# Kernel tuning notes

Hardware: AMD Instinct MI355X
Metric: run time of the kernel (lower is better)

Reference implementation:

```python
import jax, jax.numpy as jnp
import numpy as np

OBS_LEN, PRED_LEN, N, P = 8, 12, 4096, 32
EH, DH, EMB, BOT, NZ = 64, 128, 64, 1024, 8


def setup_inputs() -> dict:
    key = jax.random.key(0)
    ks = iter(jax.random.split(key, 64))
    rn = lambda shp, s=0.05: (jax.random.normal(next(ks), shp, jnp.float32) * s)
    d = {
        'obs_traj': rn((OBS_LEN, N, 2), 1.0),
        'obs_traj_rel': rn((OBS_LEN, N, 2), 0.5),
        'obs_speed': jax.random.uniform(next(ks), (OBS_LEN, N, 1), jnp.float32),
        'noise': rn((N, NZ), 1.0),
        'enc_emb_W': rn((2, EMB)), 'enc_emb_b': jnp.zeros((EMB,), jnp.float32),
        'enc_Wih': rn((EMB, 4 * EH)), 'enc_Whh': rn((EH, 4 * EH)), 'enc_b': jnp.zeros((4 * EH,), jnp.float32),
        'pool_sp_W': rn((2, 64)), 'pool_sp_b': jnp.zeros((64,), jnp.float32),
        'pool_spd_W': rn((1, 64)), 'pool_spd_b': jnp.zeros((64,), jnp.float32),
        'pool_l1_W': rn((192, 512)), 'pool_l1_b': jnp.zeros((512,), jnp.float32),
        'pool_bn1_g': jnp.ones((512,), jnp.float32), 'pool_bn1_b': jnp.zeros((512,), jnp.float32),
        'pool_l2_W': rn((512, BOT)), 'pool_l2_b': jnp.zeros((BOT,), jnp.float32),
        'pool_bn2_g': jnp.ones((BOT,), jnp.float32), 'pool_bn2_b': jnp.zeros((BOT,), jnp.float32),
        'spd_emb_W': rn((OBS_LEN, 64)), 'spd_emb_b': jnp.zeros((64,), jnp.float32),
        'ctx_l1_W': rn((EH + BOT + 64, 1024)), 'ctx_l1_b': jnp.zeros((1024,), jnp.float32),
        'ctx_bn1_g': jnp.ones((1024,), jnp.float32), 'ctx_bn1_b': jnp.zeros((1024,), jnp.float32),
        'ctx_l2_W': rn((1024, DH - NZ)), 'ctx_l2_b': jnp.zeros((DH - NZ,), jnp.float32),
        'ctx_bn2_g': jnp.ones((DH - NZ,), jnp.float32), 'ctx_bn2_b': jnp.zeros((DH - NZ,), jnp.float32),
        'dec_emb_W': rn((3, EMB)), 'dec_emb_b': jnp.zeros((EMB,), jnp.float32),
        'dec_Wih': rn((EMB, 4 * DH)), 'dec_Whh': rn((DH, 4 * DH)), 'dec_b': jnp.zeros((4 * DH,), jnp.float32),
        'h2p_W': rn((DH, 2)), 'h2p_b': jnp.zeros((2,), jnp.float32),
        'group_size': P,
    }
    return d


def _lstm(xs, Wih, Whh, b, h0, c0):
    # xs: [T, B, in]; PyTorch gate order (i, f, g, o)
    def step(carry, x):
        h, c = carry
        g = x @ Wih + h @ Whh + b
        i, f, gg, o = jnp.split(g, 4, axis=-1)
        c = jax.nn.sigmoid(f) * c + jax.nn.sigmoid(i) * jnp.tanh(gg)
        h = jax.nn.sigmoid(o) * jnp.tanh(c)
        return (h, c), h
    (h, c), _ = jax.lax.scan(step, (h0, c0), xs)
    return h, c


def _bn(x, g, b):
    # BatchNorm1d, eval mode with running_mean=0, running_var=1
    return x * g + b


def reference(obs_traj, obs_traj_rel, obs_speed, noise,
              enc_emb_W, enc_emb_b, enc_Wih, enc_Whh, enc_b,
              pool_sp_W, pool_sp_b, pool_spd_W, pool_spd_b,
              pool_l1_W, pool_l1_b, pool_bn1_g, pool_bn1_b,
              pool_l2_W, pool_l2_b, pool_bn2_g, pool_bn2_b,
              spd_emb_W, spd_emb_b,
              ctx_l1_W, ctx_l1_b, ctx_bn1_g, ctx_bn1_b,
              ctx_l2_W, ctx_l2_b, ctx_bn2_g, ctx_bn2_b,
              dec_emb_W, dec_emb_b, dec_Wih, dec_Whh, dec_b,
              h2p_W, h2p_b, group_size):
    n = obs_traj.shape[1]
    G = n // group_size
    # ---- Encoder: embed rel traj, run LSTM, take final hidden ----
    emb = obs_traj_rel @ enc_emb_W + enc_emb_b                       # [T, N, 64]
    h0 = jnp.zeros((n, EH), emb.dtype)
    final_h, _ = _lstm(emb, enc_Wih, enc_Whh, enc_b, h0, h0)         # [N, 64]
    # ---- PoolHiddenNet (vectorized per-group P x P social pooling) ----
    end_pos = obs_traj[-1].reshape(G, group_size, 2)                 # [G, P, 2]
    end_spd = obs_speed[-1].reshape(G, group_size, 1)                # [G, P, 1]
    hG = final_h.reshape(G, group_size, EH)                          # [G, P, 64]
    # rel[g, i, j] = pos[g, j] - pos[g, i]
    rel = end_pos[:, None, :, :] - end_pos[:, :, None, :]            # [G, P, P, 2]
    rel_e = rel @ pool_sp_W + pool_sp_b                              # [G, P, P, 64]
    spd_e = end_spd @ pool_spd_W + pool_spd_b                        # [G, P, 64]
    Pn = group_size
    feat = jnp.concatenate([
        rel_e,
        jnp.broadcast_to(hG[:, None, :, :], (G, Pn, Pn, EH)),
        jnp.broadcast_to(spd_e[:, None, :, :], (G, Pn, Pn, 64)),
    ], axis=-1)                                                      # [G, P, P, 192]
    h1 = jax.nn.relu(_bn(feat @ pool_l1_W + pool_l1_b, pool_bn1_g, pool_bn1_b))
    h2 = jax.nn.relu(_bn(h1 @ pool_l2_W + pool_l2_b, pool_bn2_g, pool_bn2_b))
    pool_h = jnp.max(h2, axis=2).reshape(n, BOT)                     # max over j -> [N, 1024]
    # ---- speed context: sigmoid(Linear(8 -> 64)) over obs speed history ----
    spd_hist = jnp.transpose(obs_speed[:, :, 0])                     # [N, 8]
    speed_ctx = jax.nn.sigmoid(spd_hist @ spd_emb_W + spd_emb_b)     # [N, 64]
    # ---- mlp_decoder_context + ped-level noise ----
    ctx_in = jnp.concatenate([final_h, pool_h, speed_ctx], axis=1)   # [N, 1152]
    c1 = jax.nn.relu(_bn(ctx_in @ ctx_l1_W + ctx_l1_b, ctx_bn1_g, ctx_bn1_b))
    ctx = jax.nn.relu(_bn(c1 @ ctx_l2_W + ctx_l2_b, ctx_bn2_g, ctx_bn2_b))  # [N, 120]
    dec_h = jnp.concatenate([ctx, noise], axis=1)                    # [N, 128]
    dec_c = jnp.zeros_like(dec_h)
    # ---- Decoder rollout (pred_len steps) ----
    last_pos = obs_traj[-1]
    last_speed = obs_speed[-1]                                       # [N, 1]
    x0 = jnp.concatenate([obs_traj_rel[-1], last_speed], axis=1) @ dec_emb_W + dec_emb_b

    def step(carry, _):
        h, c, x, lp = carry
        g = x @ dec_Wih + h @ dec_Whh + dec_b
        i, f, gg, o = jnp.split(g, 4, axis=-1)
        c = jax.nn.sigmoid(f) * c + jax.nn.sigmoid(i) * jnp.tanh(gg)
        h = jax.nn.sigmoid(o) * jnp.tanh(c)
        rel_pos = h @ h2p_W + h2p_b                                  # [N, 2]
        cur = rel_pos + lp
        x = jnp.concatenate([rel_pos, last_speed], axis=1) @ dec_emb_W + dec_emb_b
        return (h, c, x, cur), rel_pos

    _, rels = jax.lax.scan(step, (dec_h, dec_c, x0, last_pos), None, length=PRED_LEN)
    return rels  # [pred_len, N, 2]
```

## Files before the change

### kernel.cpp

```cpp
#include <hip/hip_runtime.h>

typedef __attribute__((ext_vector_type(8))) short v8s;
typedef __attribute__((ext_vector_type(4))) float v4f;
typedef unsigned short u16;

#define DINL static __device__ __forceinline__

DINL float b2f(u16 u){ union { unsigned uu; float ff; } x; x.uu = ((unsigned)u)<<16; return x.ff; }
DINL u16 f2b(float f){ union { float ff; unsigned uu; } x; x.ff = f; unsigned r = x.uu + 0x7FFFu + ((x.uu>>16)&1u); return (u16)(r>>16); }
DINL u16 f2b_hu(float f){ union { float ff; unsigned uu; } x; x.ff = f; return (u16)((x.uu + 0x8000u)>>16); }
DINL float sigm(float x){ return 1.0f/(1.0f+__expf(-x)); }
DINL float tanh_(float x){ return 2.0f/(1.0f+__expf(-2.0f*x)) - 1.0f; }
DINL float ld(const void* p, int i, int isf){
    return isf ? ((const float*)p)[i] : b2f(((const u16*)p)[i]);
}
DINL void g2lds16(const u16* g, u16* l){
    __builtin_amdgcn_global_load_lds(
        (const __attribute__((address_space(1))) unsigned int*)g,
        (__attribute__((address_space(3))) unsigned int*)l, 16, 0, 0);
}
DINL int detect_isf(const void* obs_speed){
    const u16* p = (const u16*)obs_speed;
    int f = 0;
    for (int i = 0; i < 16; ++i){
        u16 v = p[2*i];
        if ((v & 0x8000u) || v > 0x3F80u) f = 1;
    }
    return f;
}

#define FLAG_OFF 0x000000
#define AUX_OFF  0x000100
#define ENCF_OFF 0x010000
#define DECF_OFF 0x020000
#define CW2T_OFF 0x050000
#define W2T_OFF  0x090000
#define DECH_OFF 0x090000
#define CW1T_OFF 0x190000
#define IT_OFF   0x3D0000
#define IR_OFF   0x3F0000
#define IS_OFF   0x410000
#define INZ_OFF  0x420000
#define IW1H_OFF 0x430000
#define SM_OFF   0x440000
#define CTX_OFF  0x450000
#define AV_OFF   0xD50000
#define BIG_NEED 0x1550000

#define SM_EEW 0
#define SM_EEB 128
#define SM_ENB 192
#define SM_DEW 448
#define SM_DEB 640
#define SM_DNB 704
#define SM_H2W 1216
#define SM_H2B 1472
#define SM_SEW 1536
#define SM_SEB 2048

DINL void trans_tile(const void* in, u16* out, int K, int N, int isf,
                     int bx, int by, int t, float tile[64][65])
{
    const int nbase = bx*64, kbase = by*64;
    const int c = t & 63, r0 = (t >> 6)*16;
    for (int rep = 0; rep < 16; ++rep){
        int r = r0 + rep;
        int n = nbase + c;
        float v = 0.f;
        if (n < N) v = ld(in, (kbase + r)*N + n, isf);
        tile[r][c] = v;
    }
    __syncthreads();
    for (int rep = 0; rep < 16; ++rep){
        int r = r0 + rep;
        out[(size_t)(nbase + r)*K + kbase + c] = f2b(tile[c][r]);
    }
}

__global__ __launch_bounds__(256) void k_prep(
    const void* obs_traj, const void* obs_rel, const void* obs_speed, const void* noise,
    const void* eeW, const void* eeB, const void* enc_Wih, const void* enc_Whh, const void* encB,
    const void* spW, const void* spB, const void* spdW, const void* spdB,
    const void* pool_l1_W, const void* l1B, const void* bn1g, const void* bn1b,
    const void* pool_l2_W, const void* l2b, const void* bn2g, const void* bn2b,
    const void* seW, const void* seB,
    const void* ctx_l1_W, const void* c1b, const void* cbn1g, const void* cbn1b,
    const void* ctx_l2_W, const void* c2b, const void* cbn2g, const void* cbn2b,
    const void* deW, const void* deB, const void* dec_Wih, const void* dec_Whh, const void* decB,
    const void* h2W, const void* h2B,
    int* flag, float* AUX,
    u16* IT, u16* IR, u16* IS, u16* INZ, u16* IW1H, u16* SM,
    u16* W2T, u16* cW1T, u16* cW2T, u16* encF, u16* decF)
{
    __shared__ float tile[64][65];
    __shared__ int sisf;
    const int t = threadIdx.x;
    if (t == 0){
        int f = detect_isf(obs_speed);
        sisf = f;
        if (blockIdx.x == 0) *flag = f;
    }
    __syncthreads();
    const int isf = sisf;
    int bid = blockIdx.x;
    if (bid < 905){
        int idx = bid*256 + t;
        if (idx < 65536){ IT[idx] = f2b(ld(obs_traj, idx, isf)); return; }
        idx -= 65536;
        if (idx < 65536){ IR[idx] = f2b(ld(obs_rel, idx, isf)); return; }
        idx -= 65536;
        if (idx < 32768){ IS[idx] = f2b(ld(obs_speed, idx, isf)); return; }
        idx -= 32768;
        if (idx < 32768){ INZ[idx] = f2b(ld(noise, idx, isf)); return; }
        idx -= 32768;
        if (idx < 32768){ IW1H[idx] = f2b(ld(pool_l1_W, idx + 32768, isf)); return; }
        idx -= 32768;
        if (idx < 128){ SM[SM_EEW + idx] = f2b(ld(eeW, idx, isf)); return; }
        idx -= 128;
        if (idx < 64){ SM[SM_EEB + idx] = f2b(ld(eeB, idx, isf)); return; }
        idx -= 64;
        if (idx < 256){ SM[SM_ENB + idx] = f2b(ld(encB, idx, isf)); return; }
        idx -= 256;
        if (idx < 192){ SM[SM_DEW + idx] = f2b(ld(deW, idx, isf)); return; }
        idx -= 192;
        if (idx < 64){ SM[SM_DEB + idx] = f2b(ld(deB, idx, isf)); return; }
        idx -= 64;
        if (idx < 512){ SM[SM_DNB + idx] = f2b(ld(decB, idx, isf)); return; }
        idx -= 512;
        if (idx < 256){ SM[SM_H2W + idx] = f2b(ld(h2W, idx, isf)); return; }
        idx -= 256;
        if (idx < 2){ SM[SM_H2B + idx] = f2b(ld(h2B, idx, isf)); return; }
        idx -= 2;
        if (idx < 512){ SM[SM_SEW + idx] = f2b(ld(seW, idx, isf)); return; }
        idx -= 512;
        if (idx < 64){ SM[SM_SEB + idx] = f2b(ld(seB, idx, isf)); return; }
        return;
    }
    bid -= 905;
    if (bid < 512){
        int idx = bid*256 + t;
        if (idx < 32768){
            int jj = idx&7, lane = (idx>>3)&63, kcnf = idx>>9;
            int kc = kcnf&3, nf = kcnf>>2;
            int k = kc*32 + (lane>>4)*8 + jj, n = nf*16 + (lane&15);
            encF[idx] = (k < 64) ? f2b(ld(enc_Wih, k*256+n, isf)) : f2b(ld(enc_Whh, (k-64)*256+n, isf));
        } else {
            idx -= 32768;
            int jj = idx&7, lane = (idx>>3)&63, kcnf = idx>>9;
            int kc = kcnf % 6, nf = kcnf / 6;
            int k = kc*32 + (lane>>4)*8 + jj, n = nf*16 + (lane&15);
            decF[idx] = (k < 64) ? f2b(ld(dec_Wih, k*512+n, isf)) : f2b(ld(dec_Whh, (k-64)*512+n, isf));
        }
        return;
    }
    bid -= 512;
    if (bid < 128){ trans_tile(pool_l2_W, W2T, 512, 1024, isf, bid & 15, bid >> 4, t, tile); return; }
    bid -= 128;
    if (bid < 288){ trans_tile(ctx_l1_W, cW1T, 1152, 1024, isf, bid & 15, bid >> 4, t, tile); return; }
    bid -= 288;
    if (bid < 32){ trans_tile(ctx_l2_W, cW2T, 1024, 120, isf, bid & 1, bid >> 1, t, tile); return; }
    bid -= 32;
    {
        int idx = bid*256 + t;
        if (idx < 512){
            int c = idx;
            float m0 = 0.f, m1 = 0.f, qv = 0.f, cv = 0.f;
            for (int e = 0; e < 64; ++e){
                float w1a = ld(pool_l1_W, e*512 + c, isf);
                m0 += ld(spW, e, isf)*w1a;
                m1 += ld(spW, 64+e, isf)*w1a;
                cv += ld(spB, e, isf)*w1a;
                float w1c = ld(pool_l1_W, (128+e)*512 + c, isf);
                qv += ld(spdW, e, isf)*w1c;
                cv += ld(spdB, e, isf)*w1c;
            }
            cv += ld(l1B, c, isf);
            float g1 = ld(bn1g, c, isf), bb1 = ld(bn1b, c, isf);
            AUX[c] = m0; AUX[512+c] = m1; AUX[1024+c] = qv; AUX[1536+c] = cv;
            AUX[2048+c] = g1; AUX[2560+c] = bb1;
            AUX[3072+c] = g1*m0; AUX[3584+c] = g1*m1;
            return;
        }
        idx -= 512;
        if (idx < 1024){
            float g = ld(bn2g, idx, isf);
            AUX[4096+idx] = g; AUX[5120+idx] = ld(l2b, idx, isf)*g + ld(bn2b, idx, isf);
            return;
        }
        idx -= 1024;
        if (idx < 1024){
            float g = ld(cbn1g, idx, isf);
            AUX[6144+idx] = g; AUX[7168+idx] = ld(c1b, idx, isf)*g + ld(cbn1b, idx, isf);
            return;
        }
        idx -= 1024;
        if (idx < 128){
            int c = idx;
            float g  = (c < 120) ? ld(cbn2g, c, isf) : 1.f;
            float bb = (c < 120) ? (ld(c2b, c, isf)*g + ld(cbn2b, c, isf)) : 0.f;
            AUX[8192+c] = g; AUX[8320+c] = bb;
        }
    }
}

__global__ __launch_bounds__(256) void k_encoder(
    const u16* __restrict__ rel, const u16* __restrict__ embW, const u16* __restrict__ embB,
    const u16* __restrict__ encF, const u16* __restrict__ encB,
    const u16* __restrict__ IT, const u16* __restrict__ IS, const u16* __restrict__ IW1H,
    const u16* __restrict__ sW, const u16* __restrict__ sB,
    const float* __restrict__ AUX,
    u16* __restrict__ ctxIn, u16* __restrict__ Avec)
{
    __shared__ __align__(16) u16 Als[16*136];
    __shared__ float pxs[16], pys[16], sps[16];
    const int t = threadIdx.x, pedbase = blockIdx.x*16;
    const int w = t>>6, lane = t&63, quad = lane>>4, l15 = lane&15;
    for (int idx = t; idx < 16*64; idx += 256){ int p = idx>>6, jj = idx&63; Als[p*136 + 64 + jj] = 0; }
    if (t < 16){
        pxs[t] = b2f(IT[7*8192 + (pedbase+t)*2 + 0]);
        pys[t] = b2f(IT[7*8192 + (pedbase+t)*2 + 1]);
        sps[t] = b2f(IS[7*4096 + pedbase + t]);
    }
    {
        int p = t>>4, e0 = (t&15)*4;
        float rx = b2f(rel[(pedbase+p)*2 + 0]);
        float ry = b2f(rel[(pedbase+p)*2 + 1]);
        for (int e = e0; e < e0+4; ++e)
            Als[p*136 + e] = f2b(rx*b2f(embW[e]) + ry*b2f(embW[64+e]) + b2f(embB[e]));
    }
    const int j = w*16 + l15;
    const float bi = b2f(encB[j]), bff = b2f(encB[64+j]), bg = b2f(encB[128+j]), bo = b2f(encB[192+j]);
    float c4[4] = {0.f,0.f,0.f,0.f};
    for (int step = 0; step < 8; ++step){
        __syncthreads();
        v4f acc[4];
        for (int q = 0; q < 4; ++q) acc[q] = (v4f){0.f,0.f,0.f,0.f};
        for (int kc = 0; kc < 4; ++kc){
            v8s a = *(const v8s*)&Als[l15*136 + kc*32 + quad*8];
            for (int q = 0; q < 4; ++q){
                int nf = q*4 + w;
                v8s b = *(const v8s*)&encF[((nf*4 + kc)*64 + lane)*8];
                acc[q] = __builtin_amdgcn_mfma_f32_16x16x32_bf16(a, b, acc[q], 0, 0, 0);
            }
        }
        __syncthreads();
        for (int r = 0; r < 4; ++r){
            float gi = sigm(acc[0][r] + bi), gf = sigm(acc[1][r] + bff);
            float gg = tanh_(acc[2][r] + bg), go = sigm(acc[3][r] + bo);
            c4[r] = gf*c4[r] + gi*gg;
            Als[(quad*4 + r)*136 + 64 + j] = f2b(go*tanh_(c4[r]));
        }
        if (step < 7){
            int p = t>>4, e0 = (t&15)*4;
            float rx = b2f(rel[(step+1)*8192 + (pedbase+p)*2 + 0]);
            float ry = b2f(rel[(step+1)*8192 + (pedbase+p)*2 + 1]);
            for (int e = e0; e < e0+4; ++e)
                Als[p*136 + e] = f2b(rx*b2f(embW[e]) + ry*b2f(embW[64+e]) + b2f(embB[e]));
        }
    }
    __syncthreads();
    for (int idx = t; idx < 1024; idx += 256){
        int p = idx>>6, e = idx&63;
        ctxIn[(size_t)(pedbase+p)*1152 + e] = Als[p*136 + 64 + e];
    }
    {
        const int c0 = (t&127)*4, pg = (t>>7)*8;
        float4 acc[8];
        for (int p = 0; p < 8; ++p) acc[p] = make_float4(0.f,0.f,0.f,0.f);
        for (int e = 0; e < 64; ++e){
            ushort4 wv = *(const ushort4*)(IW1H + e*512 + c0);
            float w0 = b2f(wv.x), w1 = b2f(wv.y), w2 = b2f(wv.z), w3 = b2f(wv.w);
            for (int p = 0; p < 8; ++p){
                float h = b2f(Als[(pg+p)*136 + 64 + e]);
                acc[p].x += h*w0; acc[p].y += h*w1; acc[p].z += h*w2; acc[p].w += h*w3;
            }
        }
        float4 m0 = *(const float4*)(AUX + c0),        m1 = *(const float4*)(AUX + 512 + c0);
        float4 qv = *(const float4*)(AUX + 1024 + c0), cv = *(const float4*)(AUX + 1536 + c0);
        float4 g1 = *(const float4*)(AUX + 2048 + c0), bb = *(const float4*)(AUX + 2560 + c0);
        for (int p = 0; p < 8; ++p){
            float px = pxs[pg+p], py = pys[pg+p], sp = sps[pg+p];
            ushort4 o;
            o.x = f2b(g1.x*(px*m0.x + py*m1.x + sp*qv.x + cv.x + acc[p].x) + bb.x);
            o.y = f2b(g1.y*(px*m0.y + py*m1.y + sp*qv.y + cv.y + acc[p].y) + bb.y);
            o.z = f2b(g1.z*(px*m0.z + py*m1.z + sp*qv.z + cv.z + acc[p].z) + bb.z);
            o.w = f2b(g1.w*(px*m0.w + py*m1.w + sp*qv.w + cv.w + acc[p].w) + bb.w);
            *(ushort4*)&Avec[(size_t)(pedbase+pg+p)*512 + c0] = o;
        }
    }
    {
        int s = t & 63;
        for (int rep = 0; rep < 4; ++rep){
            int p = (t>>6)*4 + rep;
            int nid = pedbase + p;
            float a = b2f(sB[s]);
            for (int tt = 0; tt < 8; ++tt) a += b2f(IS[tt*4096 + nid]) * b2f(sW[tt*64 + s]);
            ctxIn[(size_t)nid*1152 + 1088 + s] = f2b(sigm(a));
        }
    }
}

__global__ __launch_bounds__(256, 2) void k_pool(
    const u16* __restrict__ Avec, const u16* __restrict__ W2T,
    const u16* __restrict__ IT, const float* __restrict__ AUX,
    u16* __restrict__ ctxIn)
{
    __shared__ __align__(16) u16 H1[64*512];
    __shared__ __align__(16) u16 Bls[128*64];
    const int t = threadIdx.x;
    const int g = blockIdx.x >> 4, ip = blockIdx.x & 15;
    const int w = t>>6, lane = t&63, quad = lane>>4, l15 = lane&15;
    const int aj = t>>3, ao = t&7;
    const float px0 = b2f(IT[7*8192 + (g*32 + ip*2 + 0)*2 + 0]);
    const float py0 = b2f(IT[7*8192 + (g*32 + ip*2 + 0)*2 + 1]);
    const float px1 = b2f(IT[7*8192 + (g*32 + ip*2 + 1)*2 + 0]);
    const float py1 = b2f(IT[7*8192 + (g*32 + ip*2 + 1)*2 + 1]);
    const float* M0G = AUX + 3072;
    const float* M1G = AUX + 3584;
    const u16* arow = Avec + (size_t)(g*32 + aj)*512 + ao*8;
    #pragma unroll
    for (int ch = 0; ch < 8; ++ch){
        union { v8s v; u16 u[8]; } av;
        av.v = *(const v8s*)(arow + ch*64);
        float a0[8], m0a[8], m1a[8];
        *(float4*)(m0a)   = *(const float4*)&M0G[ch*64 + ao*8];
        *(float4*)(m0a+4) = *(const float4*)&M0G[ch*64 + ao*8 + 4];
        *(float4*)(m1a)   = *(const float4*)&M1G[ch*64 + ao*8];
        *(float4*)(m1a+4) = *(const float4*)&M1G[ch*64 + ao*8 + 4];
        for (int i = 0; i < 8; ++i) a0[i] = b2f(av.u[i]);
        #pragma unroll
        for (int il = 0; il < 2; ++il){
            const float npx = (il == 0) ? -px0 : -px1;
            const float npy = (il == 0) ? -py0 : -py1;
            int r = il*32 + aj;
            int slot = (ch*8 + ao) ^ (r & 7);
            union { v8s v; u16 u[8]; } pk;
            for (int i = 0; i < 8; ++i){
                float v = __builtin_fmaf(npy, m1a[i], __builtin_fmaf(npx, m0a[i], a0[i]));
                pk.u[i] = f2b_hu(fmaxf(v, 0.f));
            }
            *(v8s*)&H1[r*512 + slot*8] = pk.v;
        }
    }
    const u16* bsrc = W2T + (size_t)(w*8 + (lane>>3))*512 + (size_t)((lane&7) ^ (lane>>3))*8;
    u16* bdst = &Bls[w*512];
    const float* S2 = AUX + 4096;
    const float* B2 = AUX + 5120;
    __syncthreads();
    for (int ntile = 0; ntile < 8; ++ntile){
        v4f acc[4][2];
        for (int mf = 0; mf < 4; ++mf) for (int nf = 0; nf < 2; ++nf) acc[mf][nf] = (v4f){0.f,0.f,0.f,0.f};
        const u16* bsn = bsrc + (size_t)ntile*128*512;
        for (int ch = 0; ch < 8; ++ch){
            __syncthreads();
            #pragma unroll
            for (int it = 0; it < 4; ++it)
                g2lds16(bsn + it*16384 + ch*64, bdst + it*2048);
            __syncthreads();
            #pragma unroll
            for (int kc = 0; kc < 2; ++kc){
                const int cgl = kc*4 + quad;
                v8s af[4];
                #pragma unroll
                for (int mf = 0; mf < 4; ++mf){
                    int r = mf*16 + l15;
                    int slot = ch*8 + (cgl ^ (l15 & 7));
                    af[mf] = *(const v8s*)&H1[r*512 + slot*8];
                }
                const int bslot = cgl ^ (l15 & 7);
                #pragma unroll
                for (int nf = 0; nf < 2; ++nf){
                    int col = w*32 + nf*16 + l15;
                    v8s bf = *(const v8s*)&Bls[col*64 + bslot*8];
                    acc[0][nf] = __builtin_amdgcn_mfma_f32_16x16x32_bf16(af[0], bf, acc[0][nf], 0, 0, 0);
                    acc[1][nf] = __builtin_amdgcn_mfma_f32_16x16x32_bf16(af[1], bf, acc[1][nf], 0, 0, 0);
                    acc[2][nf] = __builtin_amdgcn_mfma_f32_16x16x32_bf16(af[2], bf, acc[2][nf], 0, 0, 0);
                    acc[3][nf] = __builtin_amdgcn_mfma_f32_16x16x32_bf16(af[3], bf, acc[3][nf], 0, 0, 0);
                }
            }
        }
        for (int nf = 0; nf < 2; ++nf){
            int n = ntile*128 + w*32 + nf*16 + l15;
            float s = S2[n], bb = B2[n];
            float mm0 = 0.f, mm1 = 0.f;
            for (int mf = 0; mf < 2; ++mf) for (int r = 0; r < 4; ++r) mm0 = fmaxf(mm0, fmaxf(s*acc[mf][nf][r] + bb, 0.f));
            for (int mf = 2; mf < 4; ++mf) for (int r = 0; r < 4; ++r) mm1 = fmaxf(mm1, fmaxf(s*acc[mf][nf][r] + bb, 0.f));
            mm0 = fmaxf(mm0, __shfl_xor(mm0, 16)); mm0 = fmaxf(mm0, __shfl_xor(mm0, 32));
            mm1 = fmaxf(mm1, __shfl_xor(mm1, 16)); mm1 = fmaxf(mm1, __shfl_xor(mm1, 32));
            if (quad == 0) ctxIn[(size_t)(g*32 + ip*2 + 0)*1152 + 64 + n] = f2b(mm0);
            if (quad == 1) ctxIn[(size_t)(g*32 + ip*2 + 1)*1152 + 64 + n] = f2b(mm1);
        }
    }
}

template<int MF>
__global__ __launch_bounds__(256) void k_gemm_bt(
    const u16* __restrict__ A, int lda, const u16* __restrict__ BT,
    const float* __restrict__ S, const float* __restrict__ Bb,
    u16* __restrict__ out, int ldo, int K, int validN,
    const u16* __restrict__ noisep)
{
    __shared__ __align__(16) u16 Als[MF*32*72];
    __shared__ __align__(16) u16 Bls[128*72];
    const int t = threadIdx.x;
    const int m0 = blockIdx.x*(MF*32), n0 = blockIdx.y*128;
    const int w = t>>6, lane = t&63, quad = lane>>4, l15 = lane&15;
    const int rw = w>>1, cw = w&1;
    v4f acc[MF][4];
    for (int mf = 0; mf < MF; ++mf) for (int nf = 0; nf < 4; ++nf) acc[mf][nf] = (v4f){0.f,0.f,0.f,0.f};
    const int nch = K >> 6;
    for (int ch = 0; ch < nch; ++ch){
        const int k0 = ch*64;
        __syncthreads();
        if (MF == 4){
            const int srow = t>>1, sh = t&1;
            const u16* srcA = A + (size_t)(m0+srow)*lda + k0 + sh*32;
            u16* dstA = &Als[srow*72 + sh*32];
            ((v8s*)dstA)[0] = ((const v8s*)srcA)[0];
            ((v8s*)dstA)[1] = ((const v8s*)srcA)[1];
            ((v8s*)dstA)[2] = ((const v8s*)srcA)[2];
            ((v8s*)dstA)[3] = ((const v8s*)srcA)[3];
        } else {
            const int srow = t>>2, sh = t&3;
            const u16* srcA = A + (size_t)(m0+srow)*lda + k0 + sh*16;
            u16* dstA = &Als[srow*72 + sh*16];
            ((v8s*)dstA)[0] = ((const v8s*)srcA)[0];
            ((v8s*)dstA)[1] = ((const v8s*)srcA)[1];
        }
        {
            const int srow = t>>1, sh = t&1;
            const u16* srcB = BT + (size_t)(n0+srow)*K + k0 + sh*32;
            u16* dstB = &Bls[srow*72 + sh*32];
            ((v8s*)dstB)[0] = ((const v8s*)srcB)[0];
            ((v8s*)dstB)[1] = ((const v8s*)srcB)[1];
            ((v8s*)dstB)[2] = ((const v8s*)srcB)[2];
            ((v8s*)dstB)[3] = ((const v8s*)srcB)[3];
        }
        __syncthreads();
        for (int kc = 0; kc < 2; ++kc){
            v8s af[MF], bf[4];
            for (int mf = 0; mf < MF; ++mf) af[mf] = *(const v8s*)&Als[(rw*(MF*16) + mf*16 + l15)*72 + kc*32 + quad*8];
            for (int nf = 0; nf < 4; ++nf) bf[nf] = *(const v8s*)&Bls[(cw*64 + nf*16 + l15)*72 + kc*32 + quad*8];
            for (int mf = 0; mf < MF; ++mf)
                for (int nf = 0; nf < 4; ++nf)
                    acc[mf][nf] = __builtin_amdgcn_mfma_f32_16x16x32_bf16(af[mf], bf[nf], acc[mf][nf], 0, 0, 0);
        }
    }
    for (int nf = 0; nf < 4; ++nf){
        int n = n0 + cw*64 + nf*16 + l15;
        bool okn = (n < validN);
        float s = okn ? S[n] : 0.f, bb = okn ? Bb[n] : 0.f;
        bool okz = (!okn) && (noisep != nullptr) && (n < 128);
        for (int mf = 0; mf < MF; ++mf){
            int m = m0 + rw*(MF*16) + mf*16 + quad*4;
            for (int r = 0; r < 4; ++r){
                float v = fmaxf(s*acc[mf][nf][r] + bb, 0.f);
                if (okn) out[(size_t)(m+r)*ldo + n] = f2b(v);
                else if (okz) out[(size_t)(m+r)*ldo + n] = noisep[(size_t)(m+r)*8 + (n - 120)];
            }
        }
    }
}

__global__ __launch_bounds__(256) void k_decoder(
    const u16* __restrict__ decH0, const u16* __restrict__ decF, const u16* __restrict__ decB,
    const u16* __restrict__ dembW, const u16* __restrict__ dembB,
    const u16* __restrict__ h2pW, const u16* __restrict__ h2pB,
    const u16* __restrict__ obs_rel, const u16* __restrict__ obs_speed,
    const int* __restrict__ flag, void* __restrict__ outp)
{
    __shared__ __align__(16) u16 Als[16*200];
    __shared__ float rps[16][2];
    __shared__ float sps[16];
    __shared__ float h2ps[256];
    const int t = threadIdx.x, pedbase = blockIdx.x*16;
    const int w = t>>6, lane = t&63, quad = lane>>4, l15 = lane&15;
    const int isf = *flag;
    for (int idx = t; idx < 2048; idx += 256){
        int p = idx>>7, jj = idx&127;
        Als[p*200 + 64 + jj] = decH0[(pedbase+p)*128 + jj];
    }
    h2ps[t] = b2f(h2pW[t]);
    if (t < 16) sps[t] = b2f(obs_speed[7*4096 + pedbase + t]);
    if (t < 32){ int p = t>>1, cmp = t&1; rps[p][cmp] = b2f(obs_rel[7*8192 + (pedbase+p)*2 + cmp]); }
    __syncthreads();
    {
        int p = t>>4, e0 = (t&15)*4;
        for (int e = e0; e < e0+4; ++e){
            float v = rps[p][0]*b2f(dembW[e]) + rps[p][1]*b2f(dembW[64+e]) + sps[p]*b2f(dembW[128+e]) + b2f(dembB[e]);
            Als[p*200 + e] = f2b(v);
        }
    }
    float bI[2], bF[2], bG[2], bO[2];
    for (int nfl = 0; nfl < 2; ++nfl){
        int j = w*32 + nfl*16 + l15;
        bI[nfl] = b2f(decB[j]); bF[nfl] = b2f(decB[128+j]);
        bG[nfl] = b2f(decB[256+j]); bO[nfl] = b2f(decB[384+j]);
    }
    float c8[2][4] = {{0.f,0.f,0.f,0.f},{0.f,0.f,0.f,0.f}};
    for (int s = 0; s < 12; ++s){
        __syncthreads();
        v4f acc[4][2];
        for (int q = 0; q < 4; ++q) for (int nfl = 0; nfl < 2; ++nfl) acc[q][nfl] = (v4f){0.f,0.f,0.f,0.f};
        for (int kc = 0; kc < 6; ++kc){
            v8s a = *(const v8s*)&Als[l15*200 + kc*32 + quad*8];
            for (int q = 0; q < 4; ++q){
                for (int nfl = 0; nfl < 2; ++nfl){
                    int nf = q*8 + w*2 + nfl;
                    v8s b = *(const v8s*)&decF[((nf*6 + kc)*64 + lane)*8];
                    acc[q][nfl] = __builtin_amdgcn_mfma_f32_16x16x32_bf16(a, b, acc[q][nfl], 0, 0, 0);
                }
            }
        }
        __syncthreads();
        for (int nfl = 0; nfl < 2; ++nfl){
            int j = w*32 + nfl*16 + l15;
            for (int r = 0; r < 4; ++r){
                float gi = sigm(acc[0][nfl][r] + bI[nfl]), gf = sigm(acc[1][nfl][r] + bF[nfl]);
                float gg = tanh_(acc[2][nfl][r] + bG[nfl]), go = sigm(acc[3][nfl][r] + bO[nfl]);
                c8[nfl][r] = gf*c8[nfl][r] + gi*gg;
                Als[(quad*4 + r)*200 + 64 + j] = f2b(go*tanh_(c8[nfl][r]));
            }
        }
        __syncthreads();
        {
            int p = t>>4, cmp = (t>>3)&1, part = t&7;
            float rp = 0.f;
            int j0 = part*16;
            for (int jj = j0; jj < j0+16; ++jj)
                rp += b2f(Als[p*200 + 64 + jj]) * h2ps[jj*2 + cmp];
            rp += __shfl_xor(rp, 1);
            rp += __shfl_xor(rp, 2);
            rp += __shfl_xor(rp, 4);
            if (part == 0){
                rp += b2f(h2pB[cmp]);
                int oi = s*8192 + (pedbase+p)*2 + cmp;
                if (isf) ((float*)outp)[oi] = rp;
                else     ((u16*)outp)[oi]   = f2b(rp);
                rps[p][cmp] = rp;
            }
        }
        __syncthreads();
        {
            int p = t>>4, e0 = (t&15)*4;
            for (int e = e0; e < e0+4; ++e){
                float v = rps[p][0]*b2f(dembW[e]) + rps[p][1]*b2f(dembW[64+e]) + sps[p]*b2f(dembW[128+e]) + b2f(dembB[e]);
                Als[p*200 + e] = f2b(v);
            }
        }
    }
}

extern "C" void kernel_launch(void* const* d_in, const int* in_sizes, int n_in,
                              void* d_out, int out_size, void* d_ws, size_t ws_size,
                              hipStream_t stream)
{
    (void)in_sizes; (void)n_in; (void)out_size;
    const void* obs_traj  = d_in[0];
    const void* obs_rel   = d_in[1];
    const void* obs_speed = d_in[2];
    const void* noise     = d_in[3];
    const void* enc_emb_W = d_in[4];
    const void* enc_emb_b = d_in[5];
    const void* enc_Wih   = d_in[6];
    const void* enc_Whh   = d_in[7];
    const void* enc_b     = d_in[8];
    const void* pool_sp_W = d_in[9];
    const void* pool_sp_b = d_in[10];
    const void* pool_spd_W= d_in[11];
    const void* pool_spd_b= d_in[12];
    const void* pool_l1_W = d_in[13];
    const void* pool_l1_b = d_in[14];
    const void* pool_bn1_g= d_in[15];
    const void* pool_bn1_b= d_in[16];
    const void* pool_l2_W = d_in[17];
    const void* pool_l2_b = d_in[18];
    const void* pool_bn2_g= d_in[19];
    const void* pool_bn2_b= d_in[20];
    const void* spd_emb_W = d_in[21];
    const void* spd_emb_b = d_in[22];
    const void* ctx_l1_W  = d_in[23];
    const void* ctx_l1_b  = d_in[24];
    const void* ctx_bn1_g = d_in[25];
    const void* ctx_bn1_b = d_in[26];
    const void* ctx_l2_W  = d_in[27];
    const void* ctx_l2_b  = d_in[28];
    const void* ctx_bn2_g = d_in[29];
    const void* ctx_bn2_b = d_in[30];
    const void* dec_emb_W = d_in[31];
    const void* dec_emb_b = d_in[32];
    const void* dec_Wih   = d_in[33];
    const void* dec_Whh   = d_in[34];
    const void* dec_b     = d_in[35];
    const void* h2p_W     = d_in[36];
    const void* h2p_b     = d_in[37];

    char* ws = (char*)d_ws;
    int*   flag  = (int*)  (ws + FLAG_OFF);
    float* AUX   = (float*)(ws + AUX_OFF);
    u16*   encF  = (u16*)  (ws + ENCF_OFF);
    u16*   decF  = (u16*)  (ws + DECF_OFF);
    u16*   cW2T  = (u16*)  (ws + CW2T_OFF);
    u16*   W2T   = (u16*)  (ws + W2T_OFF);
    u16*   decH  = (u16*)  (ws + DECH_OFF);
    u16*   cW1T  = (u16*)  (ws + CW1T_OFF);
    u16*   IT    = (u16*)  (ws + IT_OFF);
    u16*   IR    = (u16*)  (ws + IR_OFF);
    u16*   IS    = (u16*)  (ws + IS_OFF);
    u16*   INZ   = (u16*)  (ws + INZ_OFF);
    u16*   IW1H  = (u16*)  (ws + IW1H_OFF);
    u16*   SM    = (u16*)  (ws + SM_OFF);
    u16*   ctxIn = (u16*)  (ws + CTX_OFF);
    u16*   Avec  = (u16*)  (ws + AV_OFF);
    u16*   c1    = (u16*)  (ws + AV_OFF);
    const bool big = (ws_size >= (size_t)BIG_NEED);

    k_prep<<<dim3(1876), dim3(256), 0, stream>>>(
        obs_traj, obs_rel, obs_speed, noise,
        enc_emb_W, enc_emb_b, enc_Wih, enc_Whh, enc_b,
        pool_sp_W, pool_sp_b, pool_spd_W, pool_spd_b,
        pool_l1_W, pool_l1_b, pool_bn1_g, pool_bn1_b,
        pool_l2_W, pool_l2_b, pool_bn2_g, pool_bn2_b,
        spd_emb_W, spd_emb_b,
        ctx_l1_W, ctx_l1_b, ctx_bn1_g, ctx_bn1_b,
        ctx_l2_W, ctx_l2_b, ctx_bn2_g, ctx_bn2_b,
        dec_emb_W, dec_emb_b, dec_Wih, dec_Whh, dec_b,
        h2p_W, h2p_b,
        flag, AUX, IT, IR, IS, INZ, IW1H, SM,
        W2T, cW1T, cW2T, encF, decF);
    k_encoder<<<dim3(256), dim3(256), 0, stream>>>(
        IR, SM + SM_EEW, SM + SM_EEB, encF, SM + SM_ENB,
        IT, IS, IW1H, SM + SM_SEW, SM + SM_SEB, AUX, ctxIn, Avec);
    k_pool<<<dim3(2048), dim3(256), 0, stream>>>(Avec, W2T, IT, AUX, ctxIn);
    if (big){
        k_gemm_bt<4><<<dim3(32, 8), dim3(256), 0, stream>>>(
            ctxIn, 1152, cW1T, AUX + 6144, AUX + 7168, c1, 1024, 1152, 1024, (const u16*)nullptr);
        k_gemm_bt<2><<<dim3(64, 1), dim3(256), 0, stream>>>(
            c1, 1024, cW2T, AUX + 8192, AUX + 8320, decH, 128, 1024, 120, INZ);
    } else {
        k_gemm_bt<4><<<dim3(16, 8), dim3(256), 0, stream>>>(
            ctxIn, 1152, cW1T, AUX + 6144, AUX + 7168, c1, 1024, 1152, 1024, (const u16*)nullptr);
        k_gemm_bt<2><<<dim3(32, 1), dim3(256), 0, stream>>>(
            c1, 1024, cW2T, AUX + 8192, AUX + 8320, decH, 128, 1024, 120, INZ);
        k_gemm_bt<4><<<dim3(16, 8), dim3(256), 0, stream>>>(
            ctxIn + (size_t)2048*1152, 1152, cW1T, AUX + 6144, AUX + 7168, c1, 1024, 1152, 1024, (const u16*)nullptr);
        k_gemm_bt<2><<<dim3(32, 1), dim3(256), 0, stream>>>(
            c1, 1024, cW2T, AUX + 8192, AUX + 8320, decH + (size_t)2048*128, 128, 1024, 120, INZ + (size_t)2048*8);
    }
    k_decoder<<<dim3(256), dim3(256), 0, stream>>>(
        decH, decF, SM + SM_DNB, SM + SM_DEW, SM + SM_DEB,
        SM + SM_H2W, SM + SM_H2B, IR, IS, flag, d_out);
}
```

Baseline: 454.5 us.

## Keep pool A-fragments in registers and double-buffer W2 tiles in LDS

The pooling kernel no longer stages the 64x512 hidden activation in LDS. Each wave computes its own 16-row A fragments directly into registers and covers all 128 output columns per tile, with a cross-wave max reduction through a small shared buffer. The W2 tile loads are double-buffered, so the next chunk's global-to-LDS copy overlaps the current MFMAs and one barrier per chunk is removed. The smaller LDS footprint allows three blocks per CU, at the cost of heavier register pressure from 16 A fragments and 8 accumulators, and an added barrier per n-tile.

```diff
diff --git a/kernel.cpp b/kernel.cpp
--- a/kernel.cpp
+++ b/kernel.cpp
@@ -300,95 +300,95 @@
     }
 }
 
-__global__ __launch_bounds__(256, 2) void k_pool(
+__global__ __launch_bounds__(256, 3) void k_pool(
     const u16* __restrict__ Avec, const u16* __restrict__ W2T,
     const u16* __restrict__ IT, const float* __restrict__ AUX,
     u16* __restrict__ ctxIn)
 {
-    __shared__ __align__(16) u16 H1[64*512];
-    __shared__ __align__(16) u16 Bls[128*64];
+    __shared__ __align__(16) u16 Bls[2][128*64];
+    __shared__ float red[4][128];
     const int t = threadIdx.x;
     const int g = blockIdx.x >> 4, ip = blockIdx.x & 15;
     const int w = t>>6, lane = t&63, quad = lane>>4, l15 = lane&15;
-    const int aj = t>>3, ao = t&7;
-    const float px0 = b2f(IT[7*8192 + (g*32 + ip*2 + 0)*2 + 0]);
-    const float py0 = b2f(IT[7*8192 + (g*32 + ip*2 + 0)*2 + 1]);
-    const float px1 = b2f(IT[7*8192 + (g*32 + ip*2 + 1)*2 + 0]);
-    const float py1 = b2f(IT[7*8192 + (g*32 + ip*2 + 1)*2 + 1]);
+    const int arowi = w*16 + l15;
+    const int pd = w >> 1;
+    const float px = b2f(IT[7*8192 + (g*32 + ip*2 + pd)*2 + 0]);
+    const float py = b2f(IT[7*8192 + (g*32 + ip*2 + pd)*2 + 1]);
     const float* M0G = AUX + 3072;
     const float* M1G = AUX + 3584;
-    const u16* arow = Avec + (size_t)(g*32 + aj)*512 + ao*8;
+    v8s afr[16];
+    {
+        const u16* arow = Avec + (size_t)(g*32 + (arowi & 31))*512;
+        const float npx = -px, npy = -py;
+        #pragma unroll
+        for (int ch = 0; ch < 8; ++ch){
+            #pragma unroll
+            for (int kc = 0; kc < 2; ++kc){
+                const int k0 = ch*64 + kc*32 + quad*8;
+                union { v8s v; u16 u[8]; } av; av.v = *(const v8s*)(arow + k0);
+                float4 m00 = *(const float4*)(M0G + k0), m01 = *(const float4*)(M0G + k0 + 4);
+                float4 m10 = *(const float4*)(M1G + k0), m11 = *(const float4*)(M1G + k0 + 4);
+                float m0a[8] = {m00.x,m00.y,m00.z,m00.w,m01.x,m01.y,m01.z,m01.w};
+                float m1a[8] = {m10.x,m10.y,m10.z,m10.w,m11.x,m11.y,m11.z,m11.w};
+                union { v8s v; u16 u[8]; } pk;
+                #pragma unroll
+                for (int i = 0; i < 8; ++i){
+                    float v = __builtin_fmaf(npy, m1a[i], __builtin_fmaf(npx, m0a[i], b2f(av.u[i])));
+                    pk.u[i] = f2b_hu(fmaxf(v, 0.f));
+                }
+                afr[ch*2+kc] = pk.v;
+            }
+        }
+    }
+    const u16* bsrc = W2T + (size_t)(w*8 + (lane>>3))*512 + (size_t)((lane&7)^(lane>>3))*8;
+    u16* bd[2] = { &Bls[0][w*512], &Bls[1][w*512] };
     #pragma unroll
-    for (int ch = 0; ch < 8; ++ch){
-        union { v8s v; u16 u[8]; } av;
-        av.v = *(const v8s*)(arow + ch*64);
-        float a0[8], m0a[8], m1a[8];
-        *(float4*)(m0a)   = *(const float4*)&M0G[ch*64 + ao*8];
-        *(float4*)(m0a+4) = *(const float4*)&M0G[ch*64 + ao*8 + 4];
-        *(float4*)(m1a)   = *(const float4*)&M1G[ch*64 + ao*8];
-        *(float4*)(m1a+4) = *(const float4*)&M1G[ch*64 + ao*8 + 4];
-        for (int i = 0; i < 8; ++i) a0[i] = b2f(av.u[i]);
-        #pragma unroll
-        for (int il = 0; il < 2; ++il){
-            const float npx = (il == 0) ? -px0 : -px1;
-            const float npy = (il == 0) ? -py0 : -py1;
-            int r = il*32 + aj;
-            int slot = (ch*8 + ao) ^ (r & 7);
-            union { v8s v; u16 u[8]; } pk;
-            for (int i = 0; i < 8; ++i){
-                float v = __builtin_fmaf(npy, m1a[i], __builtin_fmaf(npx, m0a[i], a0[i]));
-                pk.u[i] = f2b_hu(fmaxf(v, 0.f));
-            }
-            *(v8s*)&H1[r*512 + slot*8] = pk.v;
-        }
-    }
-    const u16* bsrc = W2T + (size_t)(w*8 + (lane>>3))*512 + (size_t)((lane&7) ^ (lane>>3))*8;
-    u16* bdst = &Bls[w*512];
+    for (int it2 = 0; it2 < 4; ++it2)
+        g2lds16(bsrc + it2*16384, bd[0] + it2*2048);
     const float* S2 = AUX + 4096;
     const float* B2 = AUX + 5120;
-    __syncthreads();
     for (int ntile = 0; ntile < 8; ++ntile){
-        v4f acc[4][2];
-        for (int mf = 0; mf < 4; ++mf) for (int nf = 0; nf < 2; ++nf) acc[mf][nf] = (v4f){0.f,0.f,0.f,0.f};
-        const u16* bsn = bsrc + (size_t)ntile*128*512;
+        v4f acc[8];
+        #pragma unroll
+        for (int nf = 0; nf < 8; ++nf) acc[nf] = (v4f){0.f,0.f,0.f,0.f};
         for (int ch = 0; ch < 8; ++ch){
+            const int it = ntile*8 + ch;
             __syncthreads();
-            #pragma unroll
-            for (int it = 0; it < 4; ++it)
-                g2lds16(bsn + it*16384 + ch*64, bdst + it*2048);
-            __syncthreads();
+            if (it < 63){
+                const int nxt = it + 1;
+                const u16* s = bsrc + (size_t)(nxt>>3)*65536 + (size_t)(nxt&7)*64;
+                u16* d = bd[nxt & 1];
+                #pragma unroll
+                for (int it2 = 0; it2 < 4; ++it2)
+                    g2lds16(s + it2*16384, d + it2*2048);
+            }
+            const u16* bb = &Bls[it & 1][0];
             #pragma unroll
             for (int kc = 0; kc < 2; ++kc){
-                const int cgl = kc*4 + quad;
-                v8s af[4];
+                const v8s af = afr[ch*2 + kc];
+                const int sl = ((kc*4 + quad) ^ (l15 & 7))*8;
                 #pragma unroll
-                for (int mf = 0; mf < 4; ++mf){
-                    int r = mf*16 + l15;
-                    int slot = ch*8 + (cgl ^ (l15 & 7));
-                    af[mf] = *(const v8s*)&H1[r*512 + slot*8];
+                for (int nf = 0; nf < 8; ++nf){
+                    v8s bf = *(const v8s*)&bb[(nf*16 + l15)*64 + sl];
+                    acc[nf] = __builtin_amdgcn_mfma_f32_16x16x32_bf16(af, bf, acc[nf], 0, 0, 0);
                 }
-                const int bslot = cgl ^ (l15 & 7);
-                #pragma unroll
-                for (int nf = 0; nf < 2; ++nf){
-                    int col = w*32 + nf*16 + l15;
-                    v8s bf = *(const v8s*)&Bls[col*64 + bslot*8];
-                    acc[0][nf] = __builtin_amdgcn_mfma_f32_16x16x32_bf16(af[0], bf, acc[0][nf], 0, 0, 0);
-                    acc[1][nf] = __builtin_amdgcn_mfma_f32_16x16x32_bf16(af[1], bf, acc[1][nf], 0, 0, 0);
-                    acc[2][nf] = __builtin_amdgcn_mfma_f32_16x16x32_bf16(af[2], bf, acc[2][nf], 0, 0, 0);
-                    acc[3][nf] = __builtin_amdgcn_mfma_f32_16x16x32_bf16(af[3], bf, acc[3][nf], 0, 0, 0);
-                }
-            }
-        }
-        for (int nf = 0; nf < 2; ++nf){
-            int n = ntile*128 + w*32 + nf*16 + l15;
-            float s = S2[n], bb = B2[n];
-            float mm0 = 0.f, mm1 = 0.f;
-            for (int mf = 0; mf < 2; ++mf) for (int r = 0; r < 4; ++r) mm0 = fmaxf(mm0, fmaxf(s*acc[mf][nf][r] + bb, 0.f));
-            for (int mf = 2; mf < 4; ++mf) for (int r = 0; r < 4; ++r) mm1 = fmaxf(mm1, fmaxf(s*acc[mf][nf][r] + bb, 0.f));
-            mm0 = fmaxf(mm0, __shfl_xor(mm0, 16)); mm0 = fmaxf(mm0, __shfl_xor(mm0, 32));
-            mm1 = fmaxf(mm1, __shfl_xor(mm1, 16)); mm1 = fmaxf(mm1, __shfl_xor(mm1, 32));
-            if (quad == 0) ctxIn[(size_t)(g*32 + ip*2 + 0)*1152 + 64 + n] = f2b(mm0);
-            if (quad == 1) ctxIn[(size_t)(g*32 + ip*2 + 1)*1152 + 64 + n] = f2b(mm1);
+            }
+        }
+        #pragma unroll
+        for (int nf = 0; nf < 8; ++nf){
+            int n = ntile*128 + nf*16 + l15;
+            float s = S2[n], bo = B2[n];
+            float m = 0.f;
+            for (int r = 0; r < 4; ++r) m = fmaxf(m, fmaxf(s*acc[nf][r] + bo, 0.f));
+            m = fmaxf(m, __shfl_xor(m, 16));
+            m = fmaxf(m, __shfl_xor(m, 32));
+            if (quad == 0) red[w][nf*16 + l15] = m;
+        }
+        __syncthreads();
+        {
+            int c = t & 127, pd2 = t >> 7;
+            float m = fmaxf(red[pd2*2][c], red[pd2*2 + 1][c]);
+            ctxIn[(size_t)(g*32 + ip*2 + pd2)*1152 + 64 + ntile*128 + c] = f2b(m);
         }
     }
 }
```

After: 505.6 us. 11.2% more time.
